# Kernel optimization log

Hardware: AMD Instinct MI355X
Metric: run time of the kernel (lower is better)

The kernel has to match this reference:

```python
import jax, jax.numpy as jnp
import numpy as np

N_NODES, E_TOT, E_ACT = 20000, 250000, 200000
LAT, OH = 128, 128
M0, M1, M2 = 64, 32, 16            # irreps_out: 64x0e + 32x1o + 16x2e
D_IR = M0 + 3 * M1 + 5 * M2        # 240
G = M1 + M2                        # gate scalars (48)
T0 = M0 + G                        # tp m=0 scalar channels (112)
I0, I1, I2 = 3 * M0, 3 * M1, 3 * M2  # tp input muls (center|edge|neighbor)


def _split(x, m0, m1, m2):
    e = x.shape[0]
    return (x[:, :m0],
            x[:, m0:m0 + 3 * m1].reshape(e, m1, 3),
            x[:, m0 + 3 * m1:].reshape(e, m2, 5))


def _merge(s0, s1, s2):
    e = s0.shape[0]
    return jnp.concatenate([s0, s1.reshape(e, -1), s2.reshape(e, -1)], axis=-1)


def _mlp(x, ws, bs):
    for i, (w, b) in enumerate(zip(ws, bs)):
        x = x @ w + b
        if i < len(ws) - 1:
            x = jax.nn.silu(x)
    return x


def _forward(latents, node_features, edge_features, cutoff_coeffs, edge_one_hot,
             wigner_D1, wigner_D2,
             W0, W1r, W1i, W2r, W2i, Gw, Gb,
             P0, P0b, P1, P2, Ew, Eb, ln_g, ln_b,
             A1, A1b, A2, A2b, A3, A3b,
             B1, B1b, B2, B2b, B3, B3b,
             O0, O1, O2,
             edge_index, active_edges):
    ec = edge_index[0][active_edges]
    en = edge_index[1][active_edges]
    # gather node features per edge (equivariant_norm_type='none' -> identity norms)
    nc0, nc1, nc2 = _split(node_features[ec], M0, M1, M2)
    ef0, ef1, ef2 = _split(edge_features, M0, M1, M2)
    nn0, nn1, nn2 = _split(node_features[en], M0, M1, M2)
    x0 = jnp.concatenate([nc0, ef0, nn0], -1)   # [E,192]
    x1 = jnp.concatenate([nc1, ef1, nn1], 1)    # [E,96,3]
    x2 = jnp.concatenate([nc2, ef2, nn2], 1)    # [E,48,5]
    lat_a = latents[active_edges]
    # --- SO(2) linear: rotate into edge frame, per-m mixing, latent gains, rotate back ---
    r1 = jnp.einsum('eij,euj->eui', wigner_D1, x1)
    r2 = jnp.einsum('eij,euj->eui', wigner_D2, x2)
    in0 = jnp.concatenate([x0, r1[:, :, 1], r2[:, :, 2]], -1)   # m=0 [E,336]
    o_m0 = in0 @ W0.T                                           # [E,160]
    ip1 = jnp.concatenate([r1[:, :, 2], r2[:, :, 3]], -1)       # m=+1 [E,144]
    im1 = jnp.concatenate([r1[:, :, 0], r2[:, :, 1]], -1)       # m=-1
    op1 = ip1 @ W1r.T - im1 @ W1i.T                             # [E,48]
    on1 = ip1 @ W1i.T + im1 @ W1r.T
    op2 = r2[:, :, 4] @ W2r.T - r2[:, :, 0] @ W2i.T             # [E,16]
    on2 = r2[:, :, 4] @ W2i.T + r2[:, :, 0] @ W2r.T
    g = lat_a @ Gw + Gb                                         # per-edge gains [E,224]
    o_m0 = o_m0 * g[:, :160]
    g1 = g[:, 160:208]; g2 = g[:, 208:224]
    op1 = op1 * g1; on1 = on1 * g1; op2 = op2 * g2; on2 = on2 * g2
    y0 = o_m0[:, :T0]
    y1 = jnp.stack([on1[:, :M1], o_m0[:, T0:T0 + M1], op1[:, :M1]], -1)          # [E,32,3]
    y2 = jnp.stack([on2, on1[:, M1:], o_m0[:, T0 + M1:], op1[:, M1:], op2], -1)  # [E,16,5]
    y1 = jnp.einsum('eji,euj->eui', wigner_D1, y1)
    y2 = jnp.einsum('eji,euj->eui', wigner_D2, y2)
    # --- gate activation ---
    gates = jax.nn.sigmoid(y0[:, M0:])
    z0 = jax.nn.silu(y0[:, :M0])
    z1 = y1 * gates[:, :M1, None]
    z2 = y2 * gates[:, M1:, None]
    # --- lin_post: per-l channel mixing, fan-in normalized, bias on scalars ---
    z0 = z0 @ P0.T / np.sqrt(M0) + P0b
    z1 = jnp.einsum('uv,evm->eum', P1, z1) / np.sqrt(M1)
    z2 = jnp.einsum('uv,evm->eum', P2, z2) / np.sqrt(M2)
    scalars = z0                                               # taken before weighting
    # --- E3ElementLinear: per-edge per-channel weights from latents ---
    w = lat_a @ Ew + Eb                                        # [E,112]
    z0 = z0 * w[:, :M0]
    z1 = z1 * w[:, M0:M0 + M1, None]
    z2 = z2 * w[:, M0 + M1:, None]
    new_edge = _merge(z0, z1, z2)
    # --- latent update: LN -> mlp1(ln_lat||scalars) -> mlp2(h||one_hot) -> cutoff ---
    mu = lat_a.mean(-1, keepdims=True)
    var = ((lat_a - mu) ** 2).mean(-1, keepdims=True)
    ln_lat = (lat_a - mu) * jax.lax.rsqrt(var + 1e-5) * ln_g + ln_b
    h = _mlp(jnp.concatenate([ln_lat, scalars], -1), (A1, A2, A3), (A1b, A2b, A3b))
    h = _mlp(jnp.concatenate([h, edge_one_hot], -1), (B1, B2, B3), (B1b, B2b, B3b))
    new_lat = cutoff_coeffs[active_edges][:, None] * h
    # --- residual update (res_update_params buffer = 0) ---
    u = jax.nn.sigmoid(jnp.asarray(0.0, new_edge.dtype))
    c_old = jax.lax.rsqrt(u * u + 1.0)
    c_new = u * c_old
    edge_out = c_old * edge_features + c_new * new_edge        # identity residual path
    latents_out = latents.at[active_edges].set(c_new * new_lat + c_old * lat_a)
    # --- layer one-hot tensor product (uvu with 128x0e) ---
    f0, f1, f2 = _split(edge_out, M0, M1, M2)
    s = 1.0 / np.sqrt(OH)
    t0 = f0 * (edge_one_hot @ O0.T) * s
    t1 = f1 * (edge_one_hot @ O1.T)[:, :, None] * s
    t2 = f2 * (edge_one_hot @ O2.T)[:, :, None] * s
    edge_out = edge_out + _merge(t0, t1, t2)
    return edge_out, latents_out


def setup_inputs() -> dict:
    key = jax.random.key(0)
    ks = iter(jax.random.split(key, 64))
    nrm = lambda sh, s=0.05: jax.random.normal(next(ks), sh, jnp.float32) * s
    inp = dict(
        latents=nrm((E_TOT, LAT), 1.0),
        node_features=nrm((N_NODES, D_IR), 1.0),
        edge_features=nrm((E_ACT, D_IR), 1.0),
        cutoff_coeffs=jax.random.uniform(next(ks), (E_TOT,), jnp.float32),
        edge_one_hot=jax.random.uniform(next(ks), (E_ACT, OH), jnp.float32),
        wigner_D1=nrm((E_ACT, 3, 3), 0.5),
        wigner_D2=nrm((E_ACT, 5, 5), 0.3),
        W0=nrm((160, I0 + I1 + I2)), W1r=nrm((48, 144)), W1i=nrm((48, 144)),
        W2r=nrm((16, 48)), W2i=nrm((16, 48)),
        Gw=nrm((LAT, 224)), Gb=jnp.ones((224,), jnp.float32),
        P0=nrm((M0, M0)), P0b=nrm((M0,)), P1=nrm((M1, M1)), P2=nrm((M2, M2)),
        Ew=nrm((LAT, M0 + M1 + M2)), Eb=jnp.ones((M0 + M1 + M2,), jnp.float32),
        ln_g=jnp.ones((LAT,), jnp.float32), ln_b=jnp.zeros((LAT,), jnp.float32),
        A1=nrm((LAT + M0, LAT)), A1b=nrm((LAT,)),
        A2=nrm((LAT, LAT)), A2b=nrm((LAT,)),
        A3=nrm((LAT, LAT)), A3b=nrm((LAT,)),
        B1=nrm((LAT + OH, LAT)), B1b=nrm((LAT,)),
        B2=nrm((LAT, LAT)), B2b=nrm((LAT,)),
        B3=nrm((LAT, LAT)), B3b=nrm((LAT,)),
        O0=nrm((M0, OH)), O1=nrm((M1, OH)), O2=nrm((M2, OH)),
        edge_index=jax.random.randint(next(ks), (2, E_TOT), 0, N_NODES, jnp.int32),
        active_edges=jnp.sort(jax.random.permutation(next(ks), E_TOT)[:E_ACT]).astype(jnp.int32),
    )
    return inp


def reference(latents, node_features, edge_features, cutoff_coeffs, edge_one_hot,
              wigner_D1, wigner_D2,
              W0, W1r, W1i, W2r, W2i, Gw, Gb,
              P0, P0b, P1, P2, Ew, Eb, ln_g, ln_b,
              A1, A1b, A2, A2b, A3, A3b,
              B1, B1b, B2, B2b, B3, B3b,
              O0, O1, O2, edge_index, active_edges):
    return _forward(latents, node_features, edge_features, cutoff_coeffs, edge_one_hot,
                    wigner_D1, wigner_D2,
                    W0, W1r, W1i, W2r, W2i, Gw, Gb,
                    P0, P0b, P1, P2, Ew, Eb, ln_g, ln_b,
                    A1, A1b, A2, A2b, A3, A3b,
                    B1, B1b, B2, B2b, B3, B3b,
                    O0, O1, O2, edge_index, active_edges)
```

## Files before the change

### kernel.cpp

```cpp
#include <hip/hip_runtime.h>

typedef unsigned short us_t;
typedef short bf16x8 __attribute__((ext_vector_type(8)));
typedef float f32x4 __attribute__((ext_vector_type(4)));

#define E_ACT 200000
#define E_TOT 250000
#define DIR   240
#define C_OLD 0.8944271909999159f
#define C_NEW 0.4472135954999579f
#define S_OH  0.08838834764831845f

#define WO_W0   0
#define WO_W1P  56320
#define WO_W1M  70144
#define WO_W2P  83968
#define WO_W2M  85504
#define WO_GW   87040
#define WO_EW   115712
#define WO_A1   130048
#define WO_A2   154624
#define WO_A3   171008
#define WO_B1   187392
#define WO_B2   220160
#define WO_B3   236544
#define WO_O0   252928
#define WO_O1   261120
#define WO_O2   265216
#define WO_P0T  267264
#define WO_P1T  271360
#define WO_P2T  272384
#define W_TOTAL 272896

__device__ __forceinline__ float b2f(us_t u) { return __uint_as_float(((unsigned)u) << 16); }
__device__ __forceinline__ us_t f2b(float f) {
    unsigned x = __float_as_uint(f);
    return (us_t)((x + 0x7fffu + ((x >> 16) & 1u)) >> 16);
}
__device__ __forceinline__ float sigm(float x) { return 1.0f / (1.0f + __expf(-x)); }

#define MFMA(a,b,c) __builtin_amdgcn_mfma_f32_16x16x32_bf16((a),(b),(c),0,0,0)

__global__ __launch_bounds__(256) void prep_kernel(
    const float* __restrict__ W0, const float* __restrict__ W1r, const float* __restrict__ W1i,
    const float* __restrict__ W2r, const float* __restrict__ W2i,
    const float* __restrict__ Gw, const float* __restrict__ Ew,
    const float* __restrict__ A1, const float* __restrict__ A2, const float* __restrict__ A3,
    const float* __restrict__ B1, const float* __restrict__ B2, const float* __restrict__ B3,
    const float* __restrict__ O0, const float* __restrict__ O1, const float* __restrict__ O2,
    const float* __restrict__ P0w, const float* __restrict__ P1w, const float* __restrict__ P2w,
    us_t* __restrict__ wb)
{
    int idx = blockIdx.x * 256 + threadIdx.x;
    if (idx >= W_TOTAL) return;
    float v;
    if (idx < WO_W1P) {
        int r = idx, n = r / 352, k = r % 352;
        v = (k < 336) ? W0[n * 336 + k] : 0.f;
    } else if (idx < WO_W1M) {
        int r = idx - WO_W1P, n = r / 288, k = r % 288;
        v = (k < 144) ? W1r[n * 144 + k] : -W1i[n * 144 + (k - 144)];
    } else if (idx < WO_W2P) {
        int r = idx - WO_W1M, n = r / 288, k = r % 288;
        v = (k < 144) ? W1i[n * 144 + k] : W1r[n * 144 + (k - 144)];
    } else if (idx < WO_W2M) {
        int r = idx - WO_W2P, n = r / 96, k = r % 96;
        v = (k < 48) ? W2r[n * 48 + k] : -W2i[n * 48 + (k - 48)];
    } else if (idx < WO_GW) {
        int r = idx - WO_W2M, n = r / 96, k = r % 96;
        v = (k < 48) ? W2i[n * 48 + k] : W2r[n * 48 + (k - 48)];
    } else if (idx < WO_EW) {
        int r = idx - WO_GW, n = r / 128, k = r % 128;
        v = Gw[k * 224 + n];
    } else if (idx < WO_A1) {
        int r = idx - WO_EW, n = r / 128, k = r % 128;
        v = Ew[k * 112 + n];
    } else if (idx < WO_A2) {
        int r = idx - WO_A1, n = r / 192, k = r % 192;
        v = A1[k * 128 + n];
    } else if (idx < WO_A3) {
        int r = idx - WO_A2, n = r / 128, k = r % 128;
        v = A2[k * 128 + n];
    } else if (idx < WO_B1) {
        int r = idx - WO_A3, n = r / 128, k = r % 128;
        v = A3[k * 128 + n];
    } else if (idx < WO_B2) {
        int r = idx - WO_B1, n = r / 256, k = r % 256;
        v = B1[k * 128 + n];
    } else if (idx < WO_B3) {
        int r = idx - WO_B2, n = r / 128, k = r % 128;
        v = B2[k * 128 + n];
    } else if (idx < WO_O0) {
        int r = idx - WO_B3, n = r / 128, k = r % 128;
        v = B3[k * 128 + n];
    } else if (idx < WO_O1) {
        v = O0[idx - WO_O0];
    } else if (idx < WO_O2) {
        v = O1[idx - WO_O1];
    } else if (idx < WO_P0T) {
        v = O2[idx - WO_O2];
    } else if (idx < WO_P1T) {
        v = P0w[idx - WO_P0T];
    } else if (idx < WO_P2T) {
        v = P1w[idx - WO_P1T];
    } else {
        int r = idx - WO_P2T, n = r / 32, k = r % 32;
        v = (k < 16) ? P2w[n * 16 + k] : 0.f;
    }
    wb[idx] = f2b(v);
}

__device__ __forceinline__ void lat_fetch_a(const float* __restrict__ latents,
                                            const int* __restrict__ aes_l,
                                            int lane, bf16x8 a[4])
{
    const int r = lane & 15, g = lane >> 4;
    const float* lp = latents + (size_t)aes_l[r] * 128 + g * 8;
    #pragma unroll
    for (int ks = 0; ks < 4; ++ks) {
        float4 v0 = *(const float4*)(lp + ks * 32);
        float4 v1 = *(const float4*)(lp + ks * 32 + 4);
        bf16x8 av;
        av[0] = (short)f2b(v0.x); av[1] = (short)f2b(v0.y);
        av[2] = (short)f2b(v0.z); av[3] = (short)f2b(v0.w);
        av[4] = (short)f2b(v1.x); av[5] = (short)f2b(v1.y);
        av[6] = (short)f2b(v1.z); av[7] = (short)f2b(v1.w);
        a[ks] = av;
    }
}

__device__ __forceinline__ void gemmW0g32(
    const us_t* __restrict__ in0s, const us_t* __restrict__ wbase,
    const bf16x8 lA[4], const bf16x8 lB[4], const float* __restrict__ Gb,
    int nt, us_t* __restrict__ om0g, int lane)
{
    const int r = lane & 15, g = lane >> 4;
    f32x4 wa = {0.f,0.f,0.f,0.f}, wb = wa, ga = wa, gb = wa;
    const us_t* apA = in0s + r * 360 + g * 8;
    const us_t* apB = in0s + (16 + r) * 360 + g * 8;
    const us_t* wp  = wbase + WO_W0 + (size_t)(nt * 16 + r) * 352 + g * 8;
    #pragma unroll
    for (int ks = 0; ks < 11; ++ks) {
        bf16x8 b = *(const bf16x8*)(wp + ks * 32);
        wa = MFMA(*(const bf16x8*)(apA + ks * 32), b, wa);
        wb = MFMA(*(const bf16x8*)(apB + ks * 32), b, wb);
    }
    const us_t* gp = wbase + WO_GW + (size_t)(nt * 16 + r) * 128 + g * 8;
    #pragma unroll
    for (int ks = 0; ks < 4; ++ks) {
        bf16x8 b = *(const bf16x8*)(gp + ks * 32);
        ga = MFMA(lA[ks], b, ga);
        gb = MFMA(lB[ks], b, gb);
    }
    float bi = Gb[nt * 16 + r];
    #pragma unroll
    for (int i = 0; i < 4; ++i) {
        int eA = g * 4 + i, eB = 16 + g * 4 + i;
        om0g[eA * 162 + nt * 16 + r] = f2b(wa[i] * (ga[i] + bi));
        om0g[eB * 162 + nt * 16 + r] = f2b(wb[i] * (gb[i] + bi));
    }
}

__device__ __forceinline__ void gemmW1g32(
    const us_t* __restrict__ cact1, const us_t* __restrict__ wbase,
    const bf16x8 lA[4], const bf16x8 lB[4], const float* __restrict__ Gb,
    int j, us_t* __restrict__ cp1g, us_t* __restrict__ cn1g, int lane)
{
    const int r = lane & 15, g = lane >> 4;
    f32x4 pa = {0.f,0.f,0.f,0.f}, pb = pa, ma = pa, mb = pa, ga = pa, gb = pa;
    const us_t* apA = cact1 + r * 296 + g * 8;
    const us_t* apB = cact1 + (16 + r) * 296 + g * 8;
    const us_t* wpP = wbase + WO_W1P + (size_t)(j * 16 + r) * 288 + g * 8;
    const us_t* wpM = wbase + WO_W1M + (size_t)(j * 16 + r) * 288 + g * 8;
    #pragma unroll
    for (int ks = 0; ks < 9; ++ks) {
        bf16x8 aA = *(const bf16x8*)(apA + ks * 32);
        bf16x8 aB = *(const bf16x8*)(apB + ks * 32);
        bf16x8 bP = *(const bf16x8*)(wpP + ks * 32);
        bf16x8 bM = *(const bf16x8*)(wpM + ks * 32);
        pa = MFMA(aA, bP, pa); pb = MFMA(aB, bP, pb);
        ma = MFMA(aA, bM, ma); mb = MFMA(aB, bM, mb);
    }
    const us_t* gp = wbase + WO_GW + (size_t)(160 + j * 16 + r) * 128 + g * 8;
    #pragma unroll
    for (int ks = 0; ks < 4; ++ks) {
        bf16x8 b = *(const bf16x8*)(gp + ks * 32);
        ga = MFMA(lA[ks], b, ga);
        gb = MFMA(lB[ks], b, gb);
    }
    float bi = Gb[160 + j * 16 + r];
    #pragma unroll
    for (int i = 0; i < 4; ++i) {
        int eA = g * 4 + i, eB = 16 + g * 4 + i;
        float gA = ga[i] + bi, gB = gb[i] + bi;
        cp1g[eA * 50 + j * 16 + r] = f2b(pa[i] * gA);
        cn1g[eA * 50 + j * 16 + r] = f2b(ma[i] * gA);
        cp1g[eB * 50 + j * 16 + r] = f2b(pb[i] * gB);
        cn1g[eB * 50 + j * 16 + r] = f2b(mb[i] * gB);
    }
}

__device__ __forceinline__ void gemmW2g32(
    const us_t* __restrict__ cact2, const us_t* __restrict__ wbase,
    const bf16x8 lA[4], const bf16x8 lB[4], const float* __restrict__ Gb,
    us_t* __restrict__ cp2g, us_t* __restrict__ cn2g, int lane)
{
    const int r = lane & 15, g = lane >> 4;
    f32x4 pa = {0.f,0.f,0.f,0.f}, pb = pa, ma = pa, mb = pa, ga = pa, gb = pa;
    const us_t* apA = cact2 + r * 104 + g * 8;
    const us_t* apB = cact2 + (16 + r) * 104 + g * 8;
    const us_t* wpP = wbase + WO_W2P + (size_t)r * 96 + g * 8;
    const us_t* wpM = wbase + WO_W2M + (size_t)r * 96 + g * 8;
    #pragma unroll
    for (int ks = 0; ks < 3; ++ks) {
        bf16x8 aA = *(const bf16x8*)(apA + ks * 32);
        bf16x8 aB = *(const bf16x8*)(apB + ks * 32);
        bf16x8 bP = *(const bf16x8*)(wpP + ks * 32);
        bf16x8 bM = *(const bf16x8*)(wpM + ks * 32);
        pa = MFMA(aA, bP, pa); pb = MFMA(aB, bP, pb);
        ma = MFMA(aA, bM, ma); mb = MFMA(aB, bM, mb);
    }
    const us_t* gp = wbase + WO_GW + (size_t)(208 + r) * 128 + g * 8;
    #pragma unroll
    for (int ks = 0; ks < 4; ++ks) {
        bf16x8 b = *(const bf16x8*)(gp + ks * 32);
        ga = MFMA(lA[ks], b, ga);
        gb = MFMA(lB[ks], b, gb);
    }
    float bi = Gb[208 + r];
    #pragma unroll
    for (int i = 0; i < 4; ++i) {
        int eA = g * 4 + i, eB = 16 + g * 4 + i;
        float gA = ga[i] + bi, gB = gb[i] + bi;
        cp2g[eA * 18 + r] = f2b(pa[i] * gA);
        cn2g[eA * 18 + r] = f2b(ma[i] * gA);
        cp2g[eB * 18 + r] = f2b(pb[i] * gB);
        cn2g[eB * 18 + r] = f2b(mb[i] * gB);
    }
}

__device__ __forceinline__ void lat_gemmE32(
    const bf16x8 lA[4], const bf16x8 lB[4],
    const us_t* __restrict__ wgt, const float* __restrict__ bias,
    int nt, us_t* __restrict__ wl, int lane)
{
    const int r = lane & 15, g = lane >> 4;
    f32x4 aA = {0.f,0.f,0.f,0.f}, aB = aA;
    const us_t* wp = wgt + (size_t)(nt * 16 + r) * 128 + g * 8;
    #pragma unroll
    for (int ks = 0; ks < 4; ++ks) {
        bf16x8 b = *(const bf16x8*)(wp + ks * 32);
        aA = MFMA(lA[ks], b, aA);
        aB = MFMA(lB[ks], b, aB);
    }
    float bi = bias[nt * 16 + r];
    #pragma unroll
    for (int i = 0; i < 4; ++i) {
        int eA = g * 4 + i, eB = 16 + g * 4 + i;
        wl[eA * 120 + nt * 16 + r] = f2b(aA[i] + bi);
        wl[eB * 120 + nt * 16 + r] = f2b(aB[i] + bi);
    }
}

template<int KS>
__device__ __forceinline__ void pgemm32(const us_t* __restrict__ actbase, int as,
                                        const us_t* __restrict__ wgt, int kp, int lane,
                                        f32x4& accA, f32x4& accB)
{
    const int r = lane & 15, g = lane >> 4;
    const us_t* apA = actbase + r * as + g * 8;
    const us_t* apB = actbase + (16 + r) * as + g * 8;
    const us_t* wp = wgt + (size_t)r * kp + g * 8;
    #pragma unroll
    for (int ks = 0; ks < KS; ++ks) {
        bf16x8 b = *(const bf16x8*)(wp + ks * 32);
        accA = MFMA(*(const bf16x8*)(apA + ks * 32), b, accA);
        accB = MFMA(*(const bf16x8*)(apB + ks * 32), b, accB);
    }
}

__global__ __launch_bounds__(256, 2) void k1_kernel(
    const float* __restrict__ latents,
    const float* __restrict__ node_features,
    const float* __restrict__ edge_features,
    const float* __restrict__ wD1,
    const float* __restrict__ wD2,
    const float* __restrict__ Gb,  const float* __restrict__ Eb,
    const float* __restrict__ P0b,
    const int* __restrict__ edge_index, const int* __restrict__ active_edges,
    const us_t* __restrict__ wbase,
    us_t* __restrict__ ne_ws, us_t* __restrict__ scal_ws)
{
    __shared__ __align__(16) char smem[80640];
    us_t* in0s  = (us_t*)(smem);
    us_t* cact1 = (us_t*)(smem + 23040);
    us_t* cact2 = (us_t*)(smem + 41984);
    float* D1l  = (float*)(smem + 48640);
    float* D2l  = (float*)(smem + 50176);
    int*   aes  = (int*)(smem + 53760);
    us_t* om0g  = (us_t*)(smem + 53888);
    us_t* cp1g  = (us_t*)(smem + 64256);
    us_t* cn1g  = (us_t*)(smem + 67456);
    us_t* cp2g  = (us_t*)(smem + 70656);
    us_t* cn2g  = (us_t*)(smem + 71808);
    us_t* wl    = (us_t*)(smem + 72960);
    us_t* z0l   = (us_t*)(smem);
    us_t* z1l   = (us_t*)(smem + 4608);
    us_t* z2l   = (us_t*)(smem + 11264);

    const int t  = threadIdx.x;
    const int e0 = blockIdx.x * 32;

    #pragma unroll
    for (int ep = 0; ep < 2; ++ep) {
        const int e = (t >> 4) + 16 * ep, l = t & 15;
        const int eg = e0 + e;
        const int ae = active_edges[eg];
        const int ec = edge_index[ae];
        const int en = edge_index[E_TOT + ae];
        if (l == 0) aes[e] = ae;

        float v1  = (l < 9) ? wD1[(size_t)eg * 9 + l] : 0.f;
        float v2a = wD2[(size_t)eg * 25 + l];
        float v2b = (l < 9) ? wD2[(size_t)eg * 25 + 16 + l] : 0.f;
        if (l < 9) D1l[e * 12 + l] = v1;
        D2l[e * 28 + l] = v2a;
        if (l < 9) D2l[e * 28 + 16 + l] = v2b;

        float d1[9], d2[25];
        #pragma unroll
        for (int i = 0; i < 9; ++i)  d1[i] = __shfl(v1, i, 16);
        #pragma unroll
        for (int i = 0; i < 16; ++i) d2[i] = __shfl(v2a, i, 16);
        #pragma unroll
        for (int i = 0; i < 9; ++i)  d2[16 + i] = __shfl(v2b, i, 16);

        const float* pc = node_features + (size_t)ec * DIR;
        const float* pe = edge_features + (size_t)eg * DIR;
        const float* pn = node_features + (size_t)en * DIR;
        us_t* in0 = in0s + e * 360;
        us_t* c1  = cact1 + e * 296;
        us_t* c2  = cact2 + e * 104;

        #pragma unroll
        for (int j = 0; j < 4; ++j) {
            int i = l + 16 * j;
            in0[i]       = f2b(pc[i]);
            in0[64 + i]  = f2b(pe[i]);
            in0[128 + i] = f2b(pn[i]);
        }
        in0[336 + l] = 0;

        #pragma unroll
        for (int jj = 0; jj < 6; ++jj) {
            int u = l + 16 * jj;
            int uu = u & 31;
            const float* sp = (u < 32 ? pc : (u < 64 ? pe : pn)) + 64 + uu * 3;
            float x0 = sp[0], x1 = sp[1], x2 = sp[2];
            float r0 = d1[0] * x0 + d1[1] * x1 + d1[2] * x2;
            float r1 = d1[3] * x0 + d1[4] * x1 + d1[5] * x2;
            float r2 = d1[6] * x0 + d1[7] * x1 + d1[8] * x2;
            c1[144 + u]  = f2b(r0);
            in0[192 + u] = f2b(r1);
            c1[u]        = f2b(r2);
        }
        #pragma unroll
        for (int jj = 0; jj < 3; ++jj) {
            int u = l + 16 * jj;
            int uu = u & 15;
            const float* sp = (u < 16 ? pc : (u < 32 ? pe : pn)) + 160 + uu * 5;
            float x0 = sp[0], x1 = sp[1], x2 = sp[2], x3 = sp[3], x4 = sp[4];
            float r[5];
            #pragma unroll
            for (int i = 0; i < 5; ++i)
                r[i] = d2[i * 5 + 0] * x0 + d2[i * 5 + 1] * x1 + d2[i * 5 + 2] * x2
                     + d2[i * 5 + 3] * x3 + d2[i * 5 + 4] * x4;
            c2[48 + u]   = f2b(r[0]);
            c1[240 + u]  = f2b(r[1]);
            in0[288 + u] = f2b(r[2]);
            c1[96 + u]   = f2b(r[3]);
            c2[u]        = f2b(r[4]);
        }
    }
    __syncthreads();

    {
        const int lane = t & 63, w = t >> 6;
        bf16x8 lA[4], lB[4];
        lat_fetch_a(latents, aes, lane, lA);
        lat_fetch_a(latents, aes + 16, lane, lB);
        if (w == 0) {
            gemmW0g32(in0s, wbase, lA, lB, Gb, 0, om0g, lane);
            gemmW0g32(in0s, wbase, lA, lB, Gb, 1, om0g, lane);
            gemmW0g32(in0s, wbase, lA, lB, Gb, 2, om0g, lane);
            gemmW1g32(cact1, wbase, lA, lB, Gb, 0, cp1g, cn1g, lane);
        } else if (w == 1) {
            gemmW0g32(in0s, wbase, lA, lB, Gb, 3, om0g, lane);
            gemmW0g32(in0s, wbase, lA, lB, Gb, 4, om0g, lane);
            gemmW0g32(in0s, wbase, lA, lB, Gb, 5, om0g, lane);
            gemmW1g32(cact1, wbase, lA, lB, Gb, 1, cp1g, cn1g, lane);
        } else if (w == 2) {
            gemmW0g32(in0s, wbase, lA, lB, Gb, 6, om0g, lane);
            gemmW0g32(in0s, wbase, lA, lB, Gb, 7, om0g, lane);
            gemmW0g32(in0s, wbase, lA, lB, Gb, 8, om0g, lane);
            gemmW1g32(cact1, wbase, lA, lB, Gb, 2, cp1g, cn1g, lane);
        } else {
            gemmW0g32(in0s, wbase, lA, lB, Gb, 9, om0g, lane);
            gemmW2g32(cact2, wbase, lA, lB, Gb, cp2g, cn2g, lane);
            #pragma unroll
            for (int nt = 0; nt < 7; ++nt)
                lat_gemmE32(lA, lB, wbase + WO_EW, Eb, nt, wl, lane);
        }
    }
    __syncthreads();

    #pragma unroll
    for (int ep = 0; ep < 2; ++ep) {
        const int e = (t >> 4) + 16 * ep, l = t & 15;
        const float* D1e = D1l + e * 12;
        const float* D2e = D2l + e * 28;
        #pragma unroll
        for (int uu = 0; uu < 2; ++uu) {
            int u = l + uu * 16;
            float j0 = b2f(cn1g[e * 50 + u]);
            float j1 = b2f(om0g[e * 162 + 112 + u]);
            float j2 = b2f(cp1g[e * 50 + u]);
            float gate = sigm(b2f(om0g[e * 162 + 64 + u]));
            #pragma unroll
            for (int i = 0; i < 3; ++i) {
                float yr = D1e[0 * 3 + i] * j0 + D1e[1 * 3 + i] * j1 + D1e[2 * 3 + i] * j2;
                z1l[e * 104 + i * 32 + u] = f2b(yr * gate);
            }
        }
        {
            int u = l;
            float j0 = b2f(cn2g[e * 18 + u]);
            float j1 = b2f(cn1g[e * 50 + 32 + u]);
            float j2 = b2f(om0g[e * 162 + 144 + u]);
            float j3 = b2f(cp1g[e * 50 + 32 + u]);
            float j4 = b2f(cp2g[e * 18 + u]);
            float gate = sigm(b2f(om0g[e * 162 + 96 + u]));
            #pragma unroll
            for (int i = 0; i < 5; ++i) {
                float yr = D2e[0 * 5 + i] * j0 + D2e[1 * 5 + i] * j1 + D2e[2 * 5 + i] * j2
                         + D2e[3 * 5 + i] * j3 + D2e[4 * 5 + i] * j4;
                z2l[e * 168 + i * 32 + u] = f2b(yr * gate);
                z2l[e * 168 + i * 32 + 16 + u] = 0;
            }
        }
        #pragma unroll
        for (int ii = 0; ii < 4; ++ii) {
            int c = l + 16 * ii;
            float v = b2f(om0g[e * 162 + c]);
            z0l[e * 72 + c] = f2b(v * sigm(v));
        }
    }
    __syncthreads();

    {
        const int lane = t & 63, w = t >> 6;
        const int r = lane & 15, g = lane >> 4;
        const float sc1 = 0.17677669529663687f;
        if (w < 2) {
            #pragma unroll
            for (int jj = 0; jj < 2; ++jj) {
                int nt = 2 * w + jj;
                f32x4 aA = {0.f,0.f,0.f,0.f}, aB = aA;
                pgemm32<2>(z0l, 72, wbase + WO_P0T + nt * 16 * 64, 64, lane, aA, aB);
                int n = nt * 16 + r;
                float bi = P0b[n];
                #pragma unroll
                for (int i = 0; i < 4; ++i) {
                    int eA = g * 4 + i, eB = 16 + g * 4 + i;
                    float zA = aA[i] * 0.125f + bi;
                    float zB = aB[i] * 0.125f + bi;
                    scal_ws[(size_t)(e0 + eA) * 64 + n] = f2b(zA);
                    scal_ws[(size_t)(e0 + eB) * 64 + n] = f2b(zB);
                    ne_ws[(size_t)(e0 + eA) * 240 + n] = f2b(zA * b2f(wl[eA * 120 + n]));
                    ne_ws[(size_t)(e0 + eB) * 240 + n] = f2b(zB * b2f(wl[eB * 120 + n]));
                }
            }
        } else if (w == 2) {
            #pragma unroll
            for (int m = 0; m < 3; ++m) {
                #pragma unroll
                for (int nt = 0; nt < 2; ++nt) {
                    f32x4 aA = {0.f,0.f,0.f,0.f}, aB = aA;
                    pgemm32<1>(z1l + m * 32, 104, wbase + WO_P1T + nt * 16 * 32, 32,
                               lane, aA, aB);
                    int u = nt * 16 + r;
                    #pragma unroll
                    for (int i = 0; i < 4; ++i) {
                        int eA = g * 4 + i, eB = 16 + g * 4 + i;
                        ne_ws[(size_t)(e0 + eA) * 240 + 64 + u * 3 + m] =
                            f2b(aA[i] * sc1 * b2f(wl[eA * 120 + 64 + u]));
                        ne_ws[(size_t)(e0 + eB) * 240 + 64 + u * 3 + m] =
                            f2b(aB[i] * sc1 * b2f(wl[eB * 120 + 64 + u]));
                    }
                }
            }
        } else if (w == 3) {
            #pragma unroll
            for (int m = 0; m < 5; ++m) {
                f32x4 aA = {0.f,0.f,0.f,0.f}, aB = aA;
                pgemm32<1>(z2l + m * 32, 168, wbase + WO_P2T, 32, lane, aA, aB);
                int u = r;
                #pragma unroll
                for (int i = 0; i < 4; ++i) {
                    int eA = g * 4 + i, eB = 16 + g * 4 + i;
                    ne_ws[(size_t)(e0 + eA) * 240 + 160 + u * 5 + m] =
                        f2b(aA[i] * 0.25f * b2f(wl[eA * 120 + 96 + u]));
                    ne_ws[(size_t)(e0 + eB) * 240 + 160 + u * 5 + m] =
                        f2b(aB[i] * 0.25f * b2f(wl[eB * 120 + 96 + u]));
                }
            }
        }
    }
}

template<int KS, bool SILU>
__device__ __forceinline__ void mlayer(
    const us_t* __restrict__ actA, const us_t* __restrict__ actB, int split, int as,
    const us_t* __restrict__ wgt, int kp, const float* __restrict__ bias,
    us_t* __restrict__ out, int os, int lane, int w)
{
    const int r = lane & 15, g = lane >> 4;
    const int n0 = 2 * w * 16, n1 = n0 + 16;
    f32x4 a00 = {0.f,0.f,0.f,0.f}, a01 = a00, a10 = a00, a11 = a00;
    const us_t* wp0 = wgt + (size_t)(n0 + r) * kp + g * 8;
    const us_t* wp1 = wgt + (size_t)(n1 + r) * kp + g * 8;
    #pragma unroll
    for (int ks = 0; ks < KS; ++ks) {
        const us_t* ab = (ks < split) ? (actA + ks * 32) : (actB + (ks - split) * 32);
        bf16x8 f0 = *(const bf16x8*)(ab + r * as + g * 8);
        bf16x8 f1 = *(const bf16x8*)(ab + (16 + r) * as + g * 8);
        bf16x8 b0 = *(const bf16x8*)(wp0 + ks * 32);
        bf16x8 b1 = *(const bf16x8*)(wp1 + ks * 32);
        a00 = MFMA(f0, b0, a00); a01 = MFMA(f0, b1, a01);
        a10 = MFMA(f1, b0, a10); a11 = MFMA(f1, b1, a11);
    }
    float bi0 = bias[n0 + r], bi1 = bias[n1 + r];
    #pragma unroll
    for (int i = 0; i < 4; ++i) {
        int eA = g * 4 + i, eB = 16 + g * 4 + i;
        float v;
        v = a00[i] + bi0; if (SILU) v *= sigm(v); out[eA * os + n0 + r] = f2b(v);
        v = a01[i] + bi1; if (SILU) v *= sigm(v); out[eA * os + n1 + r] = f2b(v);
        v = a10[i] + bi0; if (SILU) v *= sigm(v); out[eB * os + n0 + r] = f2b(v);
        v = a11[i] + bi1; if (SILU) v *= sigm(v); out[eB * os + n1 + r] = f2b(v);
    }
}

__global__ __launch_bounds__(256, 3) void k2_kernel(
    const float* __restrict__ latents, const float* __restrict__ cutoff,
    const float* __restrict__ one_hot,
    const float* __restrict__ ln_g, const float* __restrict__ ln_b,
    const float* __restrict__ A1b, const float* __restrict__ A2b, const float* __restrict__ A3b,
    const float* __restrict__ B1b, const float* __restrict__ B2b, const float* __restrict__ B3b,
    const int* __restrict__ active_edges,
    const us_t* __restrict__ wbase,
    const us_t* __restrict__ scal_ws, us_t* __restrict__ ohw_ws,
    float* __restrict__ out_lat)
{
    __shared__ __align__(16) char smem[39424];
    us_t* x_lds = (us_t*)(smem);
    us_t* h_a   = (us_t*)(smem + 12800);
    us_t* h_b   = (us_t*)(smem + 21504);
    us_t* ohl   = (us_t*)(smem + 30208);
    int*  aes_l = (int*)(smem + 38912);
    float* cut_l= (float*)(smem + 39040);

    const int t  = threadIdx.x;
    const int e0 = blockIdx.x * 32;
    const int lane = t & 63, w = t >> 6;

    {
        int ee = t >> 3, l8 = t & 7;
        int ae = active_edges[e0 + ee];
        if (l8 == 0) { aes_l[ee] = ae; cut_l[ee] = cutoff[ae]; }
        const float* lp = latents + (size_t)ae * 128 + l8 * 16;
        float xs[16];
        #pragma unroll
        for (int q = 0; q < 4; ++q) {
            float4 v = *(const float4*)(lp + q * 4);
            xs[q * 4 + 0] = v.x; xs[q * 4 + 1] = v.y;
            xs[q * 4 + 2] = v.z; xs[q * 4 + 3] = v.w;
        }
        float s1 = 0.f, s2 = 0.f;
        #pragma unroll
        for (int i = 0; i < 16; ++i) { s1 += xs[i]; s2 += xs[i] * xs[i]; }
        #pragma unroll
        for (int off = 1; off < 8; off <<= 1) {
            s1 += __shfl_xor(s1, off, 8);
            s2 += __shfl_xor(s2, off, 8);
        }
        float mu  = s1 * (1.f / 128.f);
        float var = s2 * (1.f / 128.f) - mu * mu;
        float rstd = rsqrtf(var + 1e-5f);
        #pragma unroll
        for (int i = 0; i < 16; ++i) {
            int li = l8 * 16 + i;
            x_lds[ee * 200 + li] = f2b((xs[i] - mu) * rstd * ln_g[li] + ln_b[li]);
        }
    }
    for (int idx = t; idx < 32 * 16; idx += 256) {
        int ee = idx >> 4, j = idx & 15;
        *(ushort4*)&x_lds[ee * 200 + 128 + j * 4] =
            *(const ushort4*)&scal_ws[(size_t)(e0 + ee) * 64 + j * 4];
    }
    for (int idx = t; idx < 32 * 32; idx += 256) {
        int ee = idx >> 5, j = idx & 31;
        float4 ov = *(const float4*)&one_hot[(size_t)(e0 + ee) * 128 + j * 4];
        ushort4 s; s.x = f2b(ov.x); s.y = f2b(ov.y); s.z = f2b(ov.z); s.w = f2b(ov.w);
        *(ushort4*)&ohl[ee * 136 + j * 4] = s;
    }
    __syncthreads();

    mlayer<6, true>(x_lds, x_lds, 6, 200, wbase + WO_A1, 192, A1b, h_a, 136, lane, w);
    __syncthreads();
    mlayer<4, true>(h_a, h_a, 4, 136, wbase + WO_A2, 128, A2b, h_b, 136, lane, w);
    __syncthreads();
    mlayer<4, false>(h_b, h_b, 4, 136, wbase + WO_A3, 128, A3b, h_a, 136, lane, w);
    __syncthreads();
    mlayer<8, true>(h_a, ohl, 4, 136, wbase + WO_B1, 256, B1b, h_b, 136, lane, w);
    __syncthreads();
    mlayer<4, true>(h_b, h_b, 4, 136, wbase + WO_B2, 128, B2b, h_a, 136, lane, w);
    __syncthreads();
    {
        const int r = lane & 15, g = lane >> 4;
        const int n0 = 2 * w * 16, n1 = n0 + 16;
        f32x4 a00 = {0.f,0.f,0.f,0.f}, a01 = a00, a10 = a00, a11 = a00;
        const us_t* wp0 = wbase + WO_B3 + (size_t)(n0 + r) * 128 + g * 8;
        const us_t* wp1 = wbase + WO_B3 + (size_t)(n1 + r) * 128 + g * 8;
        #pragma unroll
        for (int ks = 0; ks < 4; ++ks) {
            bf16x8 f0 = *(const bf16x8*)(h_a + ks * 32 + r * 136 + g * 8);
            bf16x8 f1 = *(const bf16x8*)(h_a + ks * 32 + (16 + r) * 136 + g * 8);
            bf16x8 b0 = *(const bf16x8*)(wp0 + ks * 32);
            bf16x8 b1 = *(const bf16x8*)(wp1 + ks * 32);
            a00 = MFMA(f0, b0, a00); a01 = MFMA(f0, b1, a01);
            a10 = MFMA(f1, b0, a10); a11 = MFMA(f1, b1, a11);
        }
        float bi0 = B3b[n0 + r], bi1 = B3b[n1 + r];
        #pragma unroll
        for (int i = 0; i < 4; ++i) {
            int eA = g * 4 + i, eB = 16 + g * 4 + i;
            int aeA = aes_l[eA], aeB = aes_l[eB];
            float cA = C_NEW * cut_l[eA], cB = C_NEW * cut_l[eB];
            float* oA = out_lat + (size_t)aeA * 128;
            float* oB = out_lat + (size_t)aeB * 128;
            const float* lA = latents + (size_t)aeA * 128;
            const float* lB = latents + (size_t)aeB * 128;
            oA[n0 + r] = cA * (a00[i] + bi0) + C_OLD * lA[n0 + r];
            oA[n1 + r] = cA * (a01[i] + bi1) + C_OLD * lA[n1 + r];
            oB[n0 + r] = cB * (a10[i] + bi0) + C_OLD * lB[n0 + r];
            oB[n1 + r] = cB * (a11[i] + bi1) + C_OLD * lB[n1 + r];
        }
    }

    {
        const int r = lane & 15, g = lane >> 4;
        const int cnt = (w == 3) ? 1 : 2;
        #pragma unroll
        for (int ii = 0; ii < 2; ++ii) {
            if (ii >= cnt) break;
            int nt = (ii == 0) ? w : w + 4;
            const us_t* wb2 = (nt < 4) ? (wbase + WO_O0 + (size_t)nt * 16 * 128)
                            : (nt < 6) ? (wbase + WO_O1 + (size_t)(nt - 4) * 16 * 128)
                                       : (wbase + WO_O2);
            f32x4 c0 = {0.f,0.f,0.f,0.f}, c1 = c0;
            const us_t* wp = wb2 + (size_t)r * 128 + g * 8;
            #pragma unroll
            for (int ks = 0; ks < 4; ++ks) {
                bf16x8 f0 = *(const bf16x8*)(ohl + ks * 32 + r * 136 + g * 8);
                bf16x8 f1 = *(const bf16x8*)(ohl + ks * 32 + (16 + r) * 136 + g * 8);
                bf16x8 b = *(const bf16x8*)(wp + ks * 32);
                c0 = MFMA(f0, b, c0); c1 = MFMA(f1, b, c1);
            }
            int n = nt * 16 + r;
            #pragma unroll
            for (int i = 0; i < 4; ++i) {
                int eA = e0 + g * 4 + i, eB = e0 + 16 + g * 4 + i;
                ohw_ws[(size_t)eA * 112 + n] = f2b(c0[i]);
                ohw_ws[(size_t)eB * 112 + n] = f2b(c1[i]);
            }
        }
    }
}

__global__ __launch_bounds__(256) void kfin_kernel(
    const float* __restrict__ edge_features, const us_t* __restrict__ ne_ws,
    const us_t* __restrict__ ohw_ws, float* __restrict__ out_edge)
{
    int idx = blockIdx.x * 256 + threadIdx.x;
    if (idx >= E_ACT * 60) return;
    int e = idx / 60;
    int c0 = (idx - e * 60) * 4;
    float4 ef = *(const float4*)&edge_features[(size_t)e * 240 + c0];
    ushort4 nv = *(const ushort4*)&ne_ws[(size_t)e * 240 + c0];
    float nef[4] = {b2f(nv.x), b2f(nv.y), b2f(nv.z), b2f(nv.w)};
    float eff[4] = {ef.x, ef.y, ef.z, ef.w};
    float4 ov;
    float* op = &ov.x;
    #pragma unroll
    for (int j = 0; j < 4; ++j) {
        int c = c0 + j;
        int o;
        if (c < 64)       o = c;
        else if (c < 160) o = 64 + (c - 64) / 3;
        else              o = 96 + (c - 160) / 5;
        float ohv = b2f(ohw_ws[(size_t)e * 112 + o]);
        op[j] = (C_OLD * eff[j] + C_NEW * nef[j]) * (1.f + S_OH * ohv);
    }
    *(float4*)&out_edge[(size_t)e * 240 + c0] = ov;
}

extern "C" void kernel_launch(void* const* d_in, const int* in_sizes, int n_in,
                              void* d_out, int out_size, void* d_ws, size_t ws_size,
                              hipStream_t stream)
{
    const float* latents  = (const float*)d_in[0];
    const float* node_f   = (const float*)d_in[1];
    const float* edge_f   = (const float*)d_in[2];
    const float* cutoff   = (const float*)d_in[3];
    const float* one_hot  = (const float*)d_in[4];
    const float* wD1      = (const float*)d_in[5];
    const float* wD2      = (const float*)d_in[6];
    const float* W0       = (const float*)d_in[7];
    const float* W1r      = (const float*)d_in[8];
    const float* W1i      = (const float*)d_in[9];
    const float* W2r      = (const float*)d_in[10];
    const float* W2i      = (const float*)d_in[11];
    const float* Gw       = (const float*)d_in[12];
    const float* Gb       = (const float*)d_in[13];
    const float* P0w      = (const float*)d_in[14];
    const float* P0b      = (const float*)d_in[15];
    const float* P1w      = (const float*)d_in[16];
    const float* P2w      = (const float*)d_in[17];
    const float* Ew       = (const float*)d_in[18];
    const float* Eb       = (const float*)d_in[19];
    const float* ln_g     = (const float*)d_in[20];
    const float* ln_b     = (const float*)d_in[21];
    const float* A1       = (const float*)d_in[22];
    const float* A1b      = (const float*)d_in[23];
    const float* A2       = (const float*)d_in[24];
    const float* A2b      = (const float*)d_in[25];
    const float* A3       = (const float*)d_in[26];
    const float* A3b      = (const float*)d_in[27];
    const float* B1       = (const float*)d_in[28];
    const float* B1b      = (const float*)d_in[29];
    const float* B2       = (const float*)d_in[30];
    const float* B2b      = (const float*)d_in[31];
    const float* B3       = (const float*)d_in[32];
    const float* B3b      = (const float*)d_in[33];
    const float* O0       = (const float*)d_in[34];
    const float* O1       = (const float*)d_in[35];
    const float* O2       = (const float*)d_in[36];
    const int* edge_index = (const int*)d_in[37];
    const int* act_e      = (const int*)d_in[38];

    float* out_edge = (float*)d_out;
    float* out_lat  = out_edge + (size_t)E_ACT * DIR;

    us_t* ne_ws   = (us_t*)d_ws;
    us_t* ohw_ws  = ne_ws + (size_t)E_ACT * DIR;
    us_t* scal_ws = ohw_ws + (size_t)E_ACT * 112;
    us_t* wbase   = scal_ws + (size_t)E_ACT * 64;

    prep_kernel<<<dim3((W_TOTAL + 255) / 256), dim3(256), 0, stream>>>(
        W0, W1r, W1i, W2r, W2i, Gw, Ew, A1, A2, A3, B1, B2, B3,
        O0, O1, O2, P0w, P1w, P2w, wbase);

    hipMemcpyAsync(out_lat, latents, (size_t)E_TOT * 128 * sizeof(float),
                   hipMemcpyDeviceToDevice, stream);

    k1_kernel<<<dim3(E_ACT / 32), dim3(256), 0, stream>>>(
        latents, node_f, edge_f, wD1, wD2, Gb, Eb, P0b,
        edge_index, act_e, wbase, ne_ws, scal_ws);

    k2_kernel<<<dim3(E_ACT / 32), dim3(256), 0, stream>>>(
        latents, cutoff, one_hot, ln_g, ln_b,
        A1b, A2b, A3b, B1b, B2b, B3b,
        act_e, wbase, scal_ws, ohw_ws, out_lat);

    kfin_kernel<<<dim3((E_ACT * 60 + 255) / 256), dim3(256), 0, stream>>>(
        edge_f, ne_ws, ohw_ws, out_edge);
}
```

Baseline: 713.6 us.

## Fuse edge, latent MLP and finalize kernels; copy only inactive latent rows

Merges the three per-edge kernels (SO(2) linear, latent MLP and output finalization) into one kernel that passes the scalar and one-hot-weight intermediates through shared memory instead of global workspaces. The full device-to-device latent copy is replaced by a kernel that binary-searches the sorted active list and copies only rows that are not active. This removes global round-trips and two launches, and avoids writing active rows twice. In exchange the fused kernel has more work per block and longer register live ranges, the copy kernel pays for a binary search on every thread, and ne_ws is still written and re-read from global memory.

```diff
diff --git a/kernel.cpp b/kernel.cpp
--- a/kernel.cpp
+++ b/kernel.cpp
@@ -110,6 +110,27 @@
     wb[idx] = f2b(v);
 }
 
+__global__ __launch_bounds__(256) void kcopy_kernel(
+    const float* __restrict__ latents, const int* __restrict__ act,
+    float* __restrict__ out_lat)
+{
+    int idx = blockIdx.x * 256 + threadIdx.x;
+    if (idx >= E_TOT * 16) return;
+    int row = idx >> 4, part = idx & 15;
+    int lo = 0, hi = E_ACT;
+    while (lo < hi) {
+        int mid = (lo + hi) >> 1;
+        if (act[mid] < row) lo = mid + 1; else hi = mid;
+    }
+    bool active = (lo < E_ACT) && (act[lo] == row);
+    if (!active) {
+        const float4* src = (const float4*)&latents[(size_t)row * 128 + part * 8];
+        float4* dst = (float4*)&out_lat[(size_t)row * 128 + part * 8];
+        dst[0] = src[0];
+        dst[1] = src[1];
+    }
+}
+
 __device__ __forceinline__ void lat_fetch_a(const float* __restrict__ latents,
                                             const int* __restrict__ aes_l,
                                             int lane, bf16x8 a[4])
@@ -279,22 +300,69 @@
     }
 }
 
-__global__ __launch_bounds__(256, 2) void k1_kernel(
+template<int KS, bool SILU>
+__device__ __forceinline__ void mlayer(
+    const us_t* __restrict__ actA, const us_t* __restrict__ actB, int split, int as,
+    const us_t* __restrict__ wgt, int kp, const float* __restrict__ bias,
+    us_t* __restrict__ out, int os, int lane, int w)
+{
+    const int r = lane & 15, g = lane >> 4;
+    const int n0 = 2 * w * 16, n1 = n0 + 16;
+    f32x4 a00 = {0.f,0.f,0.f,0.f}, a01 = a00, a10 = a00, a11 = a00;
+    const us_t* wp0 = wgt + (size_t)(n0 + r) * kp + g * 8;
+    const us_t* wp1 = wgt + (size_t)(n1 + r) * kp + g * 8;
+    #pragma unroll
+    for (int ks = 0; ks < KS; ++ks) {
+        const us_t* ab = (ks < split) ? (actA + ks * 32) : (actB + (ks - split) * 32);
+        bf16x8 f0 = *(const bf16x8*)(ab + r * as + g * 8);
+        bf16x8 f1 = *(const bf16x8*)(ab + (16 + r) * as + g * 8);
+        bf16x8 b0 = *(const bf16x8*)(wp0 + ks * 32);
+        bf16x8 b1 = *(const bf16x8*)(wp1 + ks * 32);
+        a00 = MFMA(f0, b0, a00); a01 = MFMA(f0, b1, a01);
+        a10 = MFMA(f1, b0, a10); a11 = MFMA(f1, b1, a11);
+    }
+    float bi0 = bias[n0 + r], bi1 = bias[n1 + r];
+    #pragma unroll
+    for (int i = 0; i < 4; ++i) {
+        int eA = g * 4 + i, eB = 16 + g * 4 + i;
+        float v;
+        v = a00[i] + bi0; if (SILU) v *= sigm(v); out[eA * os + n0 + r] = f2b(v);
+        v = a01[i] + bi1; if (SILU) v *= sigm(v); out[eA * os + n1 + r] = f2b(v);
+        v = a10[i] + bi0; if (SILU) v *= sigm(v); out[eB * os + n0 + r] = f2b(v);
+        v = a11[i] + bi1; if (SILU) v *= sigm(v); out[eB * os + n1 + r] = f2b(v);
+    }
+}
+
+__global__ __launch_bounds__(256, 2) void fused_kernel(
     const float* __restrict__ latents,
     const float* __restrict__ node_features,
     const float* __restrict__ edge_features,
+    const float* __restrict__ cutoff,
+    const float* __restrict__ one_hot,
     const float* __restrict__ wD1,
     const float* __restrict__ wD2,
     const float* __restrict__ Gb,  const float* __restrict__ Eb,
     const float* __restrict__ P0b,
+    const float* __restrict__ ln_g, const float* __restrict__ ln_b,
+    const float* __restrict__ A1b, const float* __restrict__ A2b, const float* __restrict__ A3b,
+    const float* __restrict__ B1b, const float* __restrict__ B2b, const float* __restrict__ B3b,
     const int* __restrict__ edge_index, const int* __restrict__ active_edges,
     const us_t* __restrict__ wbase,
-    us_t* __restrict__ ne_ws, us_t* __restrict__ scal_ws)
+    us_t* __restrict__ ne_ws,
+    float* __restrict__ out_edge, float* __restrict__ out_lat)
 {
     __shared__ __align__(16) char smem[80640];
     us_t* in0s  = (us_t*)(smem);
     us_t* cact1 = (us_t*)(smem + 23040);
     us_t* cact2 = (us_t*)(smem + 41984);
+    us_t* z0l   = (us_t*)(smem);
+    us_t* z1l   = (us_t*)(smem + 4608);
+    us_t* z2l   = (us_t*)(smem + 11264);
+    us_t* x_lds = (us_t*)(smem);
+    us_t* h_a   = (us_t*)(smem + 12800);
+    us_t* h_b   = (us_t*)(smem + 21504);
+    us_t* ohl   = (us_t*)(smem + 30208);
+    us_t* ohw_l = (us_t*)(smem + 38912);
     float* D1l  = (float*)(smem + 48640);
     float* D2l  = (float*)(smem + 50176);
     int*   aes  = (int*)(smem + 53760);
@@ -304,12 +372,12 @@
     us_t* cp2g  = (us_t*)(smem + 70656);
     us_t* cn2g  = (us_t*)(smem + 71808);
     us_t* wl    = (us_t*)(smem + 72960);
-    us_t* z0l   = (us_t*)(smem);
-    us_t* z1l   = (us_t*)(smem + 4608);
-    us_t* z2l   = (us_t*)(smem + 11264);
+    us_t* scal_l= (us_t*)(smem + 64256);
+    float* cut_l= (float*)(smem + 53888);
 
     const int t  = threadIdx.x;
     const int e0 = blockIdx.x * 32;
+    const int lane = t & 63, w = t >> 6;
 
     #pragma unroll
     for (int ep = 0; ep < 2; ++ep) {
@@ -385,7 +453,6 @@
     __syncthreads();
 
     {
-        const int lane = t & 63, w = t >> 6;
         bf16x8 lA[4], lB[4];
         lat_fetch_a(latents, aes, lane, lA);
         lat_fetch_a(latents, aes + 16, lane, lB);
@@ -458,7 +525,6 @@
     __syncthreads();
 
     {
-        const int lane = t & 63, w = t >> 6;
         const int r = lane & 15, g = lane >> 4;
         const float sc1 = 0.17677669529663687f;
         if (w < 2) {
@@ -474,8 +540,8 @@
                     int eA = g * 4 + i, eB = 16 + g * 4 + i;
                     float zA = aA[i] * 0.125f + bi;
                     float zB = aB[i] * 0.125f + bi;
-                    scal_ws[(size_t)(e0 + eA) * 64 + n] = f2b(zA);
-                    scal_ws[(size_t)(e0 + eB) * 64 + n] = f2b(zB);
+                    scal_l[eA * 64 + n] = f2b(zA);
+                    scal_l[eB * 64 + n] = f2b(zB);
                     ne_ws[(size_t)(e0 + eA) * 240 + n] = f2b(zA * b2f(wl[eA * 120 + n]));
                     ne_ws[(size_t)(e0 + eB) * 240 + n] = f2b(zB * b2f(wl[eB * 120 + n]));
                 }
@@ -516,68 +582,12 @@
             }
         }
     }
-}
-
-template<int KS, bool SILU>
-__device__ __forceinline__ void mlayer(
-    const us_t* __restrict__ actA, const us_t* __restrict__ actB, int split, int as,
-    const us_t* __restrict__ wgt, int kp, const float* __restrict__ bias,
-    us_t* __restrict__ out, int os, int lane, int w)
-{
-    const int r = lane & 15, g = lane >> 4;
-    const int n0 = 2 * w * 16, n1 = n0 + 16;
-    f32x4 a00 = {0.f,0.f,0.f,0.f}, a01 = a00, a10 = a00, a11 = a00;
-    const us_t* wp0 = wgt + (size_t)(n0 + r) * kp + g * 8;
-    const us_t* wp1 = wgt + (size_t)(n1 + r) * kp + g * 8;
-    #pragma unroll
-    for (int ks = 0; ks < KS; ++ks) {
-        const us_t* ab = (ks < split) ? (actA + ks * 32) : (actB + (ks - split) * 32);
-        bf16x8 f0 = *(const bf16x8*)(ab + r * as + g * 8);
-        bf16x8 f1 = *(const bf16x8*)(ab + (16 + r) * as + g * 8);
-        bf16x8 b0 = *(const bf16x8*)(wp0 + ks * 32);
-        bf16x8 b1 = *(const bf16x8*)(wp1 + ks * 32);
-        a00 = MFMA(f0, b0, a00); a01 = MFMA(f0, b1, a01);
-        a10 = MFMA(f1, b0, a10); a11 = MFMA(f1, b1, a11);
-    }
-    float bi0 = bias[n0 + r], bi1 = bias[n1 + r];
-    #pragma unroll
-    for (int i = 0; i < 4; ++i) {
-        int eA = g * 4 + i, eB = 16 + g * 4 + i;
-        float v;
-        v = a00[i] + bi0; if (SILU) v *= sigm(v); out[eA * os + n0 + r] = f2b(v);
-        v = a01[i] + bi1; if (SILU) v *= sigm(v); out[eA * os + n1 + r] = f2b(v);
-        v = a10[i] + bi0; if (SILU) v *= sigm(v); out[eB * os + n0 + r] = f2b(v);
-        v = a11[i] + bi1; if (SILU) v *= sigm(v); out[eB * os + n1 + r] = f2b(v);
-    }
-}
-
-__global__ __launch_bounds__(256, 3) void k2_kernel(
-    const float* __restrict__ latents, const float* __restrict__ cutoff,
-    const float* __restrict__ one_hot,
-    const float* __restrict__ ln_g, const float* __restrict__ ln_b,
-    const float* __restrict__ A1b, const float* __restrict__ A2b, const float* __restrict__ A3b,
-    const float* __restrict__ B1b, const float* __restrict__ B2b, const float* __restrict__ B3b,
-    const int* __restrict__ active_edges,
-    const us_t* __restrict__ wbase,
-    const us_t* __restrict__ scal_ws, us_t* __restrict__ ohw_ws,
-    float* __restrict__ out_lat)
-{
-    __shared__ __align__(16) char smem[39424];
-    us_t* x_lds = (us_t*)(smem);
-    us_t* h_a   = (us_t*)(smem + 12800);
-    us_t* h_b   = (us_t*)(smem + 21504);
-    us_t* ohl   = (us_t*)(smem + 30208);
-    int*  aes_l = (int*)(smem + 38912);
-    float* cut_l= (float*)(smem + 39040);
-
-    const int t  = threadIdx.x;
-    const int e0 = blockIdx.x * 32;
-    const int lane = t & 63, w = t >> 6;
+    __syncthreads();
 
     {
         int ee = t >> 3, l8 = t & 7;
-        int ae = active_edges[e0 + ee];
-        if (l8 == 0) { aes_l[ee] = ae; cut_l[ee] = cutoff[ae]; }
+        int ae = aes[ee];
+        if (l8 == 0) cut_l[ee] = cutoff[ae];
         const float* lp = latents + (size_t)ae * 128 + l8 * 16;
         float xs[16];
         #pragma unroll
@@ -602,11 +612,12 @@
             int li = l8 * 16 + i;
             x_lds[ee * 200 + li] = f2b((xs[i] - mu) * rstd * ln_g[li] + ln_b[li]);
         }
-    }
-    for (int idx = t; idx < 32 * 16; idx += 256) {
-        int ee = idx >> 4, j = idx & 15;
-        *(ushort4*)&x_lds[ee * 200 + 128 + j * 4] =
-            *(const ushort4*)&scal_ws[(size_t)(e0 + ee) * 64 + j * 4];
+        #pragma unroll
+        for (int q = 0; q < 2; ++q) {
+            int j = l8 * 2 + q;
+            *(ushort4*)&x_lds[ee * 200 + 128 + j * 4] =
+                *(const ushort4*)&scal_l[ee * 64 + j * 4];
+        }
     }
     for (int idx = t; idx < 32 * 32; idx += 256) {
         int ee = idx >> 5, j = idx & 31;
@@ -626,6 +637,7 @@
     __syncthreads();
     mlayer<4, true>(h_b, h_b, 4, 136, wbase + WO_B2, 128, B2b, h_a, 136, lane, w);
     __syncthreads();
+
     {
         const int r = lane & 15, g = lane >> 4;
         const int n0 = 2 * w * 16, n1 = n0 + 16;
@@ -645,7 +657,7 @@
         #pragma unroll
         for (int i = 0; i < 4; ++i) {
             int eA = g * 4 + i, eB = 16 + g * 4 + i;
-            int aeA = aes_l[eA], aeB = aes_l[eB];
+            int aeA = aes[eA], aeB = aes[eB];
             float cA = C_NEW * cut_l[eA], cB = C_NEW * cut_l[eB];
             float* oA = out_lat + (size_t)aeA * 128;
             float* oB = out_lat + (size_t)aeB * 128;
@@ -657,7 +669,6 @@
             oB[n1 + r] = cB * (a11[i] + bi1) + C_OLD * lB[n1 + r];
         }
     }
-
     {
         const int r = lane & 15, g = lane >> 4;
         const int cnt = (w == 3) ? 1 : 2;
@@ -680,39 +691,36 @@
             int n = nt * 16 + r;
             #pragma unroll
             for (int i = 0; i < 4; ++i) {
-                int eA = e0 + g * 4 + i, eB = e0 + 16 + g * 4 + i;
-                ohw_ws[(size_t)eA * 112 + n] = f2b(c0[i]);
-                ohw_ws[(size_t)eB * 112 + n] = f2b(c1[i]);
+                int eA = g * 4 + i, eB = 16 + g * 4 + i;
+                ohw_l[eA * 112 + n] = f2b(c0[i]);
+                ohw_l[eB * 112 + n] = f2b(c1[i]);
             }
         }
     }
-}
-
-__global__ __launch_bounds__(256) void kfin_kernel(
-    const float* __restrict__ edge_features, const us_t* __restrict__ ne_ws,
-    const us_t* __restrict__ ohw_ws, float* __restrict__ out_edge)
-{
-    int idx = blockIdx.x * 256 + threadIdx.x;
-    if (idx >= E_ACT * 60) return;
-    int e = idx / 60;
-    int c0 = (idx - e * 60) * 4;
-    float4 ef = *(const float4*)&edge_features[(size_t)e * 240 + c0];
-    ushort4 nv = *(const ushort4*)&ne_ws[(size_t)e * 240 + c0];
-    float nef[4] = {b2f(nv.x), b2f(nv.y), b2f(nv.z), b2f(nv.w)};
-    float eff[4] = {ef.x, ef.y, ef.z, ef.w};
-    float4 ov;
-    float* op = &ov.x;
-    #pragma unroll
-    for (int j = 0; j < 4; ++j) {
-        int c = c0 + j;
-        int o;
-        if (c < 64)       o = c;
-        else if (c < 160) o = 64 + (c - 64) / 3;
-        else              o = 96 + (c - 160) / 5;
-        float ohv = b2f(ohw_ws[(size_t)e * 112 + o]);
-        op[j] = (C_OLD * eff[j] + C_NEW * nef[j]) * (1.f + S_OH * ohv);
-    }
-    *(float4*)&out_edge[(size_t)e * 240 + c0] = ov;
+    __syncthreads();
+
+    for (int idx = t; idx < 32 * 60; idx += 256) {
+        int e = idx / 60;
+        int c0 = (idx - e * 60) * 4;
+        size_t eg = (size_t)(e0 + e);
+        float4 ef = *(const float4*)&edge_features[eg * 240 + c0];
+        ushort4 nv = *(const ushort4*)&ne_ws[eg * 240 + c0];
+        float nef[4] = {b2f(nv.x), b2f(nv.y), b2f(nv.z), b2f(nv.w)};
+        float eff[4] = {ef.x, ef.y, ef.z, ef.w};
+        float4 ov;
+        float* op = &ov.x;
+        #pragma unroll
+        for (int j = 0; j < 4; ++j) {
+            int c = c0 + j;
+            int o;
+            if (c < 64)       o = c;
+            else if (c < 160) o = 64 + (c - 64) / 3;
+            else              o = 96 + (c - 160) / 5;
+            float ohv = b2f(ohw_l[e * 112 + o]);
+            op[j] = (C_OLD * eff[j] + C_NEW * nef[j]) * (1.f + S_OH * ohv);
+        }
+        *(float4*)&out_edge[eg * 240 + c0] = ov;
+    }
 }
 
 extern "C" void kernel_launch(void* const* d_in, const int* in_sizes, int n_in,
@@ -763,26 +771,18 @@
     float* out_lat  = out_edge + (size_t)E_ACT * DIR;
 
     us_t* ne_ws   = (us_t*)d_ws;
-    us_t* ohw_ws  = ne_ws + (size_t)E_ACT * DIR;
-    us_t* scal_ws = ohw_ws + (size_t)E_ACT * 112;
-    us_t* wbase   = scal_ws + (size_t)E_ACT * 64;
+    us_t* wbase   = ne_ws + (size_t)E_ACT * DIR;
 
     prep_kernel<<<dim3((W_TOTAL + 255) / 256), dim3(256), 0, stream>>>(
         W0, W1r, W1i, W2r, W2i, Gw, Ew, A1, A2, A3, B1, B2, B3,
         O0, O1, O2, P0w, P1w, P2w, wbase);
 
-    hipMemcpyAsync(out_lat, latents, (size_t)E_TOT * 128 * sizeof(float),
-                   hipMemcpyDeviceToDevice, stream);
-
-    k1_kernel<<<dim3(E_ACT / 32), dim3(256), 0, stream>>>(
-        latents, node_f, edge_f, wD1, wD2, Gb, Eb, P0b,
-        edge_index, act_e, wbase, ne_ws, scal_ws);
-
-    k2_kernel<<<dim3(E_ACT / 32), dim3(256), 0, stream>>>(
-        latents, cutoff, one_hot, ln_g, ln_b,
+    kcopy_kernel<<<dim3((E_TOT * 16 + 255) / 256), dim3(256), 0, stream>>>(
+        latents, act_e, out_lat);
+
+    fused_kernel<<<dim3(E_ACT / 32), dim3(256), 0, stream>>>(
+        latents, node_f, edge_f, cutoff, one_hot, wD1, wD2,
+        Gb, Eb, P0b, ln_g, ln_b,
         A1b, A2b, A3b, B1b, B2b, B3b,
-        act_e, wbase, scal_ws, ohw_ws, out_lat);
-
-    kfin_kernel<<<dim3((E_ACT * 60 + 255) / 256), dim3(256), 0, stream>>>(
-        edge_f, ne_ws, ohw_ws, out_edge);
-}
+        edge_index, act_e, wbase, ne_ws, out_edge, out_lat);
+}
```

After: 699.3 us, median of 3. 1.02x faster.
